# Optimization experiments

Measured on AMD Instinct MI355X. Metric: run time of the kernel, lower is better.

Reference implementation:

```python
import jax, jax.numpy as jnp
import numpy as np

N_SRC = 100000
N_DST = 20000
E = 1250000
D_IN = 64
D_OUT = 64
NEG_SLOPE = 0.2  # PyG GATConv default


def setup_inputs() -> dict:
    key = jax.random.key(0)
    ks = jax.random.split(key, 8)
    x = jax.random.normal(ks[0], (N_SRC, D_IN), dtype=jnp.float32)
    res_n_id = jax.random.randint(ks[1], (N_DST,), 0, N_SRC)
    edge_src = jax.random.randint(ks[2], (E,), 0, N_SRC)
    edge_dst = jax.random.randint(ks[3], (E,), 0, N_DST)
    W = jax.random.normal(ks[4], (D_IN, D_OUT), dtype=jnp.float32) / np.sqrt(D_IN)
    att_src = jax.random.normal(ks[5], (D_OUT,), dtype=jnp.float32)
    att_dst = jax.random.normal(ks[6], (D_OUT,), dtype=jnp.float32)
    bias = jax.random.normal(ks[7], (D_OUT,), dtype=jnp.float32) * 0.01
    return {"x": x, "res_n_id": res_n_id, "edge_src": edge_src,
            "edge_dst": edge_dst, "W": W, "att_src": att_src,
            "att_dst": att_dst, "bias": bias}


def reference(x, res_n_id, edge_src, edge_dst, W, att_src, att_dst, bias):
    # Shared linear transform (in_channels is an int -> one weight in PyG)
    h_src = x @ W                      # [N_src, D_OUT]
    h_dst = x[res_n_id] @ W            # [N_dst, D_OUT]
    # Per-node attention logits
    a_src = h_src @ att_src            # [N_src]
    a_dst = h_dst @ att_dst            # [N_dst]
    # Per-edge attention score (gather)
    e = jax.nn.leaky_relu(a_src[edge_src] + a_dst[edge_dst], NEG_SLOPE)  # [E]
    # Segment softmax over incoming edges of each destination node
    m = jax.ops.segment_max(e, edge_dst, num_segments=N_DST)             # [N_dst]
    ex = jnp.exp(e - m[edge_dst])
    denom = jax.ops.segment_sum(ex, edge_dst, num_segments=N_DST)        # [N_dst]
    alpha = ex / (denom[edge_dst] + 1e-16)                               # [E]
    # (dropout on alpha is eval-mode identity)
    # Weighted scatter-aggregate
    msg = h_src[edge_src] * alpha[:, None]                               # [E, D_OUT]
    out = jax.ops.segment_sum(msg, edge_dst, num_segments=N_DST)         # [N_dst, D_OUT]
    return out + bias
```

## Files before the change

### kernel.cpp

```cpp
#include <hip/hip_runtime.h>

#define N_SRC 100000
#define N_DST 20000
#define NE    1250000
#define D     64
#define NEG_SLOPE 0.2f

#define NBKT 2500
#define BCAP 768
#define TILE 4096

__device__ __forceinline__ unsigned short f2bf(float f) {
    unsigned u = __float_as_uint(f);
    u += 0x7FFFu + ((u >> 16) & 1);
    return (unsigned short)(u >> 16);
}
__device__ __forceinline__ float blo(unsigned u) { return __uint_as_float(u << 16); }
__device__ __forceinline__ float bhi(unsigned u) { return __uint_as_float(u & 0xFFFF0000u); }

__global__ void k_wad_init(const float* __restrict__ W,
                           const float* __restrict__ att_dst,
                           float* __restrict__ wad, int* __restrict__ gcur) {
    int g = blockIdx.x * 256 + threadIdx.x;
    if (g < NBKT) gcur[g] = g * BCAP;
    if (g < D) {
        float s = 0.f;
#pragma unroll
        for (int c = 0; c < D; ++c) s += W[g * D + c] * att_dst[c];
        wad[g] = s;
    }
}

__global__ __launch_bounds__(256) void k_h(const float* __restrict__ x,
                                           const float* __restrict__ W,
                                           const float* __restrict__ att_src,
                                           unsigned short* __restrict__ hb,
                                           float* __restrict__ a_src) {
    __shared__ float xs[64 * 68];
    __shared__ float Ws[64 * 64];
    int t = threadIdx.x;
    int row0 = blockIdx.x * 64;
    int nrows = N_SRC - row0; if (nrows > 64) nrows = 64;
    {
        const float4* W4 = (const float4*)W;
        float4* Ws4 = (float4*)Ws;
#pragma unroll
        for (int p = 0; p < 4; ++p) Ws4[t + 256 * p] = W4[t + 256 * p];
    }
#pragma unroll
    for (int p = 0; p < 4; ++p) {
        int idx = t + 256 * p;
        int r = idx >> 4, kq = idx & 15;
        float4 v = make_float4(0.f, 0.f, 0.f, 0.f);
        if (r < nrows) v = *(const float4*)(x + (size_t)(row0 + r) * D + 4 * kq);
        xs[(4 * kq + 0) * 68 + r] = v.x;
        xs[(4 * kq + 1) * 68 + r] = v.y;
        xs[(4 * kq + 2) * 68 + r] = v.z;
        xs[(4 * kq + 3) * 68 + r] = v.w;
    }
    __syncthreads();
    int ry = t >> 4, cx = t & 15;
    float acc[4][4] = {{0.f}};
#pragma unroll 8
    for (int k = 0; k < 64; ++k) {
        float4 xv = *(const float4*)(xs + k * 68 + 4 * ry);
        float4 wv = *(const float4*)(Ws + k * 64 + 4 * cx);
        acc[0][0] = fmaf(xv.x, wv.x, acc[0][0]); acc[0][1] = fmaf(xv.x, wv.y, acc[0][1]);
        acc[0][2] = fmaf(xv.x, wv.z, acc[0][2]); acc[0][3] = fmaf(xv.x, wv.w, acc[0][3]);
        acc[1][0] = fmaf(xv.y, wv.x, acc[1][0]); acc[1][1] = fmaf(xv.y, wv.y, acc[1][1]);
        acc[1][2] = fmaf(xv.y, wv.z, acc[1][2]); acc[1][3] = fmaf(xv.y, wv.w, acc[1][3]);
        acc[2][0] = fmaf(xv.z, wv.x, acc[2][0]); acc[2][1] = fmaf(xv.z, wv.y, acc[2][1]);
        acc[2][2] = fmaf(xv.z, wv.z, acc[2][2]); acc[2][3] = fmaf(xv.z, wv.w, acc[2][3]);
        acc[3][0] = fmaf(xv.w, wv.x, acc[3][0]); acc[3][1] = fmaf(xv.w, wv.y, acc[3][1]);
        acc[3][2] = fmaf(xv.w, wv.z, acc[3][2]); acc[3][3] = fmaf(xv.w, wv.w, acc[3][3]);
    }
    float4 a4 = *(const float4*)(att_src + 4 * cx);
#pragma unroll
    for (int j = 0; j < 4; ++j) {
        int r = 4 * ry + j;
        if (r < nrows) {
            ushort4 hv;
            hv.x = f2bf(acc[j][0]); hv.y = f2bf(acc[j][1]);
            hv.z = f2bf(acc[j][2]); hv.w = f2bf(acc[j][3]);
            *(ushort4*)(hb + (size_t)(row0 + r) * D + 4 * cx) = hv;
        }
        float p = acc[j][0] * a4.x + acc[j][1] * a4.y + acc[j][2] * a4.z + acc[j][3] * a4.w;
        p += __shfl_xor(p, 1, 64); p += __shfl_xor(p, 2, 64);
        p += __shfl_xor(p, 4, 64); p += __shfl_xor(p, 8, 64);
        if (cx == 0 && r < nrows) a_src[row0 + r] = p;
    }
}

__global__ __launch_bounds__(1024) void k_bucket(const int* __restrict__ es,
                                                 const int* __restrict__ ed,
                                                 int* __restrict__ gcur,
                                                 int* __restrict__ buf) {
    __shared__ int hist[NBKT];
    __shared__ int lofs[NBKT];
    __shared__ int gbase[NBKT];
    __shared__ int wtot[16];
    __shared__ int stage[TILE];
    int t = threadIdx.x;
    int w = t >> 6, lane = t & 63;
    int base = blockIdx.x * TILE;
    int nE = NE - base; if (nE > TILE) nE = TILE;

    for (int i = t; i < NBKT; i += 1024) hist[i] = 0;
    __syncthreads();

    int s_[4], d_[4], rk_[4];
#pragma unroll
    for (int j = 0; j < 4; ++j) {
        int i = t + 1024 * j;
        d_[j] = -1;
        if (i < nE) {
            s_[j] = es[base + i];
            d_[j] = ed[base + i];
            rk_[j] = atomicAdd(&hist[d_[j] >> 3], 1);
        }
    }
    __syncthreads();

    int c0 = t * 3;
    int hc[3] = {0, 0, 0};
#pragma unroll
    for (int j = 0; j < 3; ++j)
        if (c0 + j < NBKT) hc[j] = hist[c0 + j];
    int sum = hc[0] + hc[1] + hc[2];
    int incl = sum;
#pragma unroll
    for (int off = 1; off < 64; off <<= 1) {
        int u = __shfl_up(incl, off, 64);
        if (lane >= off) incl += u;
    }
    if (lane == 63) wtot[w] = incl;
    __syncthreads();
    int wpre = 0;
#pragma unroll
    for (int j = 0; j < 16; ++j) wpre += (j < w) ? wtot[j] : 0;
    {
        int run = wpre + incl - sum;
#pragma unroll
        for (int j = 0; j < 3; ++j) {
            int b = c0 + j;
            if (b < NBKT) {
                lofs[b] = run;
                gbase[b] = hc[j] ? atomicAdd(&gcur[b], hc[j]) : 0;
                run += hc[j];
            }
        }
    }
    __syncthreads();

#pragma unroll
    for (int j = 0; j < 4; ++j) {
        if (d_[j] >= 0) {
            int b = d_[j] >> 3;
            stage[lofs[b] + rk_[j]] = s_[j] | ((d_[j] & 7) << 17) | (b << 20);
        }
    }
    __syncthreads();

    for (int idx = t; idx < nE; idx += 1024) {
        int rec = stage[idx];
        int b = ((unsigned)rec) >> 20;
        int gpos = gbase[b] + idx - lofs[b];
        if (gpos < (b + 1) * BCAP) buf[gpos] = rec;
    }
}

__global__ __launch_bounds__(256) void k_aggB(const int* __restrict__ buf,
                                              const int* __restrict__ gcur,
                                              const float* __restrict__ a_src,
                                              const float* __restrict__ x,
                                              const int* __restrict__ res_n_id,
                                              const float* __restrict__ wad,
                                              const unsigned short* __restrict__ hb,
                                              const float* __restrict__ bias,
                                              float* __restrict__ out) {
    __shared__ int2 sorted[BCAP];
    __shared__ int  scw[8 * 4];
    __shared__ int  begs[9];
    int bk = blockIdx.x;
    int t = threadIdx.x;
    int w = t >> 6, lane = t & 63;
    int n = gcur[bk] - bk * BCAP;
    if (n > BCAP) n = BCAP;
    if (n < 0) n = 0;

    const int* src = buf + (size_t)bk * BCAP;
    int r0 = 0, r1 = 0, r2 = 0;
    int bin0 = -1, bin1 = -1, bin2 = -1;
    if (t < n)       { r0 = src[t];       bin0 = (r0 >> 17) & 7; }
    if (t + 256 < n) { r1 = src[t + 256]; bin1 = (r1 >> 17) & 7; }
    if (t + 512 < n) { r2 = src[t + 512]; bin2 = (r2 >> 17) & 7; }

    int h[8], incl[8];
#pragma unroll
    for (int i = 0; i < 8; ++i)
        h[i] = (bin0 == i) + (bin1 == i) + (bin2 == i);

#pragma unroll
    for (int i = 0; i < 8; ++i) {
        int v = h[i];
#pragma unroll
        for (int off = 1; off < 64; off <<= 1) {
            int u = __shfl_up(v, off, 64);
            if (lane >= off) v += u;
        }
        incl[i] = v;
        int tot = __shfl(v, 63, 64);
        if (lane == 0) scw[i * 4 + w] = tot;
    }
    __syncthreads();

    if (t < 32) {
        int v = scw[t];
#pragma unroll
        for (int off = 1; off < 32; off <<= 1) {
            int u = __shfl_up(v, off, 64);
            if (t >= off) v += u;
        }
        scw[t] = v;
    }
    __syncthreads();
    if (t < 8) begs[t] = (t == 0) ? 0 : scw[t * 4 - 1];
    if (t == 8) begs[8] = n;

    int p0 = 0, p1 = 0, p2 = 0;
#pragma unroll
    for (int i = 0; i < 8; ++i) {
        int idx = i * 4 + w;
        int base_i = ((idx ? scw[idx - 1] : 0)) + (incl[i] - h[i]);
        p0 += (bin0 == i) ? base_i : 0;
        p1 += (bin1 == i) ? base_i : 0;
        p2 += (bin2 == i) ? base_i : 0;
    }
    p1 += (bin1 == bin0);
    p2 += (bin2 == bin0) + (bin2 == bin1);
    if (bin0 >= 0) sorted[p0].x = r0;
    if (bin1 >= 0) sorted[p1].x = r1;
    if (bin2 >= 0) sorted[p2].x = r2;
    float wv = wad[lane];
    __syncthreads();

    int g = lane >> 3, il = lane & 7;
    float4 bA = *(const float4*)(bias + 8 * il);
    float4 bB = *(const float4*)(bias + 8 * il + 4);
#pragma unroll
    for (int q = 0; q < 2; ++q) {
        int dlo = w * 2 + q;
        int beg = begs[dlo], end = begs[dlo + 1];

        int xrow = res_n_id[bk * 8 + dlo];
        float ad = x[(size_t)xrow * D + lane] * wv;
#pragma unroll
        for (int off = 32; off; off >>= 1) ad += __shfl_xor(ad, off, 64);

        float mx = -1e30f;
        for (int i = beg + lane; i < end; i += 64) {
            int meta = sorted[i].x;
            float v = a_src[meta & 0x1FFFF] + ad;
            v = v > 0.f ? v : NEG_SLOPE * v;
            sorted[i].y = __float_as_int(v);
            mx = fmaxf(mx, v);
        }
#pragma unroll
        for (int off = 32; off; off >>= 1) mx = fmaxf(mx, __shfl_xor(mx, off, 64));
        __builtin_amdgcn_wave_barrier();

        float a0 = 0.f, a1 = 0.f, a2 = 0.f, a3 = 0.f;
        float a4c = 0.f, a5 = 0.f, a6 = 0.f, a7 = 0.f;
        float den = 0.f;
        int i = beg;
        for (; i + 32 <= end; i += 32) {
            int2 ra = sorted[i + g];
            int2 rb = sorted[i + 8 + g];
            int2 rc = sorted[i + 16 + g];
            int2 rd = sorted[i + 24 + g];
            const uint4 ha = *(const uint4*)(hb + (size_t)(ra.x & 0x1FFFF) * D + 8 * il);
            const uint4 hc4 = *(const uint4*)(hb + (size_t)(rb.x & 0x1FFFF) * D + 8 * il);
            const uint4 he = *(const uint4*)(hb + (size_t)(rc.x & 0x1FFFF) * D + 8 * il);
            const uint4 hf = *(const uint4*)(hb + (size_t)(rd.x & 0x1FFFF) * D + 8 * il);
            float ea = __expf(__int_as_float(ra.y) - mx);
            float eb = __expf(__int_as_float(rb.y) - mx);
            float ec = __expf(__int_as_float(rc.y) - mx);
            float ed = __expf(__int_as_float(rd.y) - mx);
            a0 = fmaf(ea, blo(ha.x), a0); a1 = fmaf(ea, bhi(ha.x), a1);
            a2 = fmaf(ea, blo(ha.y), a2); a3 = fmaf(ea, bhi(ha.y), a3);
            a4c = fmaf(ea, blo(ha.z), a4c); a5 = fmaf(ea, bhi(ha.z), a5);
            a6 = fmaf(ea, blo(ha.w), a6); a7 = fmaf(ea, bhi(ha.w), a7);
            a0 = fmaf(eb, blo(hc4.x), a0); a1 = fmaf(eb, bhi(hc4.x), a1);
            a2 = fmaf(eb, blo(hc4.y), a2); a3 = fmaf(eb, bhi(hc4.y), a3);
            a4c = fmaf(eb, blo(hc4.z), a4c); a5 = fmaf(eb, bhi(hc4.z), a5);
            a6 = fmaf(eb, blo(hc4.w), a6); a7 = fmaf(eb, bhi(hc4.w), a7);
            a0 = fmaf(ec, blo(he.x), a0); a1 = fmaf(ec, bhi(he.x), a1);
            a2 = fmaf(ec, blo(he.y), a2); a3 = fmaf(ec, bhi(he.y), a3);
            a4c = fmaf(ec, blo(he.z), a4c); a5 = fmaf(ec, bhi(he.z), a5);
            a6 = fmaf(ec, blo(he.w), a6); a7 = fmaf(ec, bhi(he.w), a7);
            a0 = fmaf(ed, blo(hf.x), a0); a1 = fmaf(ed, bhi(hf.x), a1);
            a2 = fmaf(ed, blo(hf.y), a2); a3 = fmaf(ed, bhi(hf.y), a3);
            a4c = fmaf(ed, blo(hf.z), a4c); a5 = fmaf(ed, bhi(hf.z), a5);
            a6 = fmaf(ed, blo(hf.w), a6); a7 = fmaf(ed, bhi(hf.w), a7);
            den += (ea + eb) + (ec + ed);
        }
        for (; i + 16 <= end; i += 16) {
            int2 ra = sorted[i + g];
            int2 rb = sorted[i + 8 + g];
            const uint4 ha = *(const uint4*)(hb + (size_t)(ra.x & 0x1FFFF) * D + 8 * il);
            const uint4 hc4 = *(const uint4*)(hb + (size_t)(rb.x & 0x1FFFF) * D + 8 * il);
            float ea = __expf(__int_as_float(ra.y) - mx);
            float eb = __expf(__int_as_float(rb.y) - mx);
            a0 = fmaf(ea, blo(ha.x), a0); a1 = fmaf(ea, bhi(ha.x), a1);
            a2 = fmaf(ea, blo(ha.y), a2); a3 = fmaf(ea, bhi(ha.y), a3);
            a4c = fmaf(ea, blo(ha.z), a4c); a5 = fmaf(ea, bhi(ha.z), a5);
            a6 = fmaf(ea, blo(ha.w), a6); a7 = fmaf(ea, bhi(ha.w), a7);
            a0 = fmaf(eb, blo(hc4.x), a0); a1 = fmaf(eb, bhi(hc4.x), a1);
            a2 = fmaf(eb, blo(hc4.y), a2); a3 = fmaf(eb, bhi(hc4.y), a3);
            a4c = fmaf(eb, blo(hc4.z), a4c); a5 = fmaf(eb, bhi(hc4.z), a5);
            a6 = fmaf(eb, blo(hc4.w), a6); a7 = fmaf(eb, bhi(hc4.w), a7);
            den += ea + eb;
        }
        for (; i < end; i += 8) {
            int idx = i + g;
            bool ok = idx < end;
            float e = 0.f;
            if (ok) {
                int2 r = sorted[idx];
                e = __expf(__int_as_float(r.y) - mx);
                const uint4 hv = *(const uint4*)(hb + (size_t)(r.x & 0x1FFFF) * D + 8 * il);
                a0 = fmaf(e, blo(hv.x), a0); a1 = fmaf(e, bhi(hv.x), a1);
                a2 = fmaf(e, blo(hv.y), a2); a3 = fmaf(e, bhi(hv.y), a3);
                a4c = fmaf(e, blo(hv.z), a4c); a5 = fmaf(e, bhi(hv.z), a5);
                a6 = fmaf(e, blo(hv.w), a6); a7 = fmaf(e, bhi(hv.w), a7);
            }
            den += e;
        }
#pragma unroll
        for (int off = 8; off <= 32; off <<= 1) {
            a0 += __shfl_xor(a0, off, 64); a1 += __shfl_xor(a1, off, 64);
            a2 += __shfl_xor(a2, off, 64); a3 += __shfl_xor(a3, off, 64);
            a4c += __shfl_xor(a4c, off, 64); a5 += __shfl_xor(a5, off, 64);
            a6 += __shfl_xor(a6, off, 64); a7 += __shfl_xor(a7, off, 64);
            den += __shfl_xor(den, off, 64);
        }
        if (g == 0) {
            float inv = 1.f / (den + 1e-16f);
            float4 oA, oB;
            oA.x = a0 * inv + bA.x; oA.y = a1 * inv + bA.y;
            oA.z = a2 * inv + bA.z; oA.w = a3 * inv + bA.w;
            oB.x = a4c * inv + bB.x; oB.y = a5 * inv + bB.y;
            oB.z = a6 * inv + bB.z; oB.w = a7 * inv + bB.w;
            float* orow = out + ((size_t)bk * 8 + dlo) * D + 8 * il;
            *(float4*)orow = oA;
            *(float4*)(orow + 4) = oB;
        }
    }
}

extern "C" void kernel_launch(void* const* d_in, const int* in_sizes, int n_in,
                              void* d_out, int out_size, void* d_ws, size_t ws_size,
                              hipStream_t stream) {
    const float* x        = (const float*)d_in[0];
    const int*   res_n_id = (const int*)d_in[1];
    const int*   edge_src = (const int*)d_in[2];
    const int*   edge_dst = (const int*)d_in[3];
    const float* W        = (const float*)d_in[4];
    const float* att_src  = (const float*)d_in[5];
    const float* att_dst  = (const float*)d_in[6];
    const float* bias     = (const float*)d_in[7];
    float* out = (float*)d_out;

    char* w = (char*)d_ws;
    unsigned short* hb = (unsigned short*)w; w += (size_t)N_SRC * D * 2;
    int*   buf   = (int*)w;   w += (size_t)NBKT * BCAP * 4;
    float* a_src = (float*)w; w += (size_t)N_SRC * 4;
    float* wad   = (float*)w; w += 256;
    int*   gcur  = (int*)w;   w += (size_t)NBKT * 4;

    k_wad_init<<<(NBKT + 255) / 256, 256, 0, stream>>>(W, att_dst, wad, gcur);
    k_h<<<(N_SRC + 63) / 64, 256, 0, stream>>>(x, W, att_src, hb, a_src);
    k_bucket<<<(NE + TILE - 1) / TILE, 1024, 0, stream>>>(edge_src, edge_dst, gcur, buf);
    k_aggB<<<NBKT, 256, 0, stream>>>(buf, gcur, a_src, x, res_n_id, wad, hb, bias, out);
}
```

Baseline: 161.3 us.

## Precompute exponentiated edge scores during bucketing and drop segment max pass

A new small kernel computes the per-destination attention logit once. The bucketing kernel then gathers a_src and a_dst for each edge, applies leaky-ReLU and exp, and stores the result next to the packed edge record as an int2. The aggregation kernel loses its per-segment max reduction, its a_src gathers and its per-edge exp, and uses the stored weights directly. In exchange the bucket buffer doubles in size, and softmax without max subtraction can overflow if logits get large.

```diff
diff --git a/kernel.cpp b/kernel.cpp
--- a/kernel.cpp
+++ b/kernel.cpp
@@ -91,15 +91,32 @@
     }
 }
 
+__global__ __launch_bounds__(256) void k_adst(const float* __restrict__ x,
+                                              const int* __restrict__ res_n_id,
+                                              const float* __restrict__ wad,
+                                              float* __restrict__ a_dst) {
+    int tid = threadIdx.x;
+    int wid = blockIdx.x * 4 + (tid >> 6);
+    int lane = tid & 63;
+    if (wid >= N_DST) return;
+    int row = res_n_id[wid];
+    float p = x[(size_t)row * D + lane] * wad[lane];
+#pragma unroll
+    for (int off = 32; off; off >>= 1) p += __shfl_xor(p, off, 64);
+    if (lane == 0) a_dst[wid] = p;
+}
+
 __global__ __launch_bounds__(1024) void k_bucket(const int* __restrict__ es,
                                                  const int* __restrict__ ed,
+                                                 const float* __restrict__ a_src,
+                                                 const float* __restrict__ a_dst,
                                                  int* __restrict__ gcur,
-                                                 int* __restrict__ buf) {
+                                                 int2* __restrict__ buf) {
     __shared__ int hist[NBKT];
     __shared__ int lofs[NBKT];
     __shared__ int gbase[NBKT];
     __shared__ int wtot[16];
-    __shared__ int stage[TILE];
+    __shared__ int2 stage[TILE];
     int t = threadIdx.x;
     int w = t >> 6, lane = t & 63;
     int base = blockIdx.x * TILE;
@@ -119,6 +136,11 @@
             rk_[j] = atomicAdd(&hist[d_[j] >> 3], 1);
         }
     }
+    float as_[4], ad_[4];
+#pragma unroll
+    for (int j = 0; j < 4; ++j) {
+        if (d_[j] >= 0) { as_[j] = a_src[s_[j]]; ad_[j] = a_dst[d_[j]]; }
+    }
     __syncthreads();
 
     int c0 = t * 3;
@@ -155,26 +177,27 @@
 #pragma unroll
     for (int j = 0; j < 4; ++j) {
         if (d_[j] >= 0) {
+            float v = as_[j] + ad_[j];
+            v = v > 0.f ? v : NEG_SLOPE * v;
+            float ex = __expf(v);
             int b = d_[j] >> 3;
-            stage[lofs[b] + rk_[j]] = s_[j] | ((d_[j] & 7) << 17) | (b << 20);
+            stage[lofs[b] + rk_[j]] =
+                make_int2(s_[j] | ((d_[j] & 7) << 17) | (b << 20),
+                          __float_as_int(ex));
         }
     }
     __syncthreads();
 
     for (int idx = t; idx < nE; idx += 1024) {
-        int rec = stage[idx];
-        int b = ((unsigned)rec) >> 20;
+        int2 rec = stage[idx];
+        int b = ((unsigned)rec.x) >> 20;
         int gpos = gbase[b] + idx - lofs[b];
         if (gpos < (b + 1) * BCAP) buf[gpos] = rec;
     }
 }
 
-__global__ __launch_bounds__(256) void k_aggB(const int* __restrict__ buf,
+__global__ __launch_bounds__(256) void k_aggB(const int2* __restrict__ buf,
                                               const int* __restrict__ gcur,
-                                              const float* __restrict__ a_src,
-                                              const float* __restrict__ x,
-                                              const int* __restrict__ res_n_id,
-                                              const float* __restrict__ wad,
                                               const unsigned short* __restrict__ hb,
                                               const float* __restrict__ bias,
                                               float* __restrict__ out) {
@@ -188,12 +211,12 @@
     if (n > BCAP) n = BCAP;
     if (n < 0) n = 0;
 
-    const int* src = buf + (size_t)bk * BCAP;
-    int r0 = 0, r1 = 0, r2 = 0;
+    const int2* src = buf + (size_t)bk * BCAP;
+    int2 r0 = make_int2(0, 0), r1 = make_int2(0, 0), r2 = make_int2(0, 0);
     int bin0 = -1, bin1 = -1, bin2 = -1;
-    if (t < n)       { r0 = src[t];       bin0 = (r0 >> 17) & 7; }
-    if (t + 256 < n) { r1 = src[t + 256]; bin1 = (r1 >> 17) & 7; }
-    if (t + 512 < n) { r2 = src[t + 512]; bin2 = (r2 >> 17) & 7; }
+    if (t < n)       { r0 = src[t];       bin0 = (r0.x >> 17) & 7; }
+    if (t + 256 < n) { r1 = src[t + 256]; bin1 = (r1.x >> 17) & 7; }
+    if (t + 512 < n) { r2 = src[t + 512]; bin2 = (r2.x >> 17) & 7; }
 
     int h[8], incl[8];
 #pragma unroll
@@ -238,10 +261,9 @@
     }
     p1 += (bin1 == bin0);
     p2 += (bin2 == bin0) + (bin2 == bin1);
-    if (bin0 >= 0) sorted[p0].x = r0;
-    if (bin1 >= 0) sorted[p1].x = r1;
-    if (bin2 >= 0) sorted[p2].x = r2;
-    float wv = wad[lane];
+    if (bin0 >= 0) sorted[p0] = r0;
+    if (bin1 >= 0) sorted[p1] = r1;
+    if (bin2 >= 0) sorted[p2] = r2;
     __syncthreads();
 
     int g = lane >> 3, il = lane & 7;
@@ -251,23 +273,6 @@
     for (int q = 0; q < 2; ++q) {
         int dlo = w * 2 + q;
         int beg = begs[dlo], end = begs[dlo + 1];
-
-        int xrow = res_n_id[bk * 8 + dlo];
-        float ad = x[(size_t)xrow * D + lane] * wv;
-#pragma unroll
-        for (int off = 32; off; off >>= 1) ad += __shfl_xor(ad, off, 64);
-
-        float mx = -1e30f;
-        for (int i = beg + lane; i < end; i += 64) {
-            int meta = sorted[i].x;
-            float v = a_src[meta & 0x1FFFF] + ad;
-            v = v > 0.f ? v : NEG_SLOPE * v;
-            sorted[i].y = __float_as_int(v);
-            mx = fmaxf(mx, v);
-        }
-#pragma unroll
-        for (int off = 32; off; off >>= 1) mx = fmaxf(mx, __shfl_xor(mx, off, 64));
-        __builtin_amdgcn_wave_barrier();
 
         float a0 = 0.f, a1 = 0.f, a2 = 0.f, a3 = 0.f;
         float a4c = 0.f, a5 = 0.f, a6 = 0.f, a7 = 0.f;
@@ -282,10 +287,10 @@
             const uint4 hc4 = *(const uint4*)(hb + (size_t)(rb.x & 0x1FFFF) * D + 8 * il);
             const uint4 he = *(const uint4*)(hb + (size_t)(rc.x & 0x1FFFF) * D + 8 * il);
             const uint4 hf = *(const uint4*)(hb + (size_t)(rd.x & 0x1FFFF) * D + 8 * il);
-            float ea = __expf(__int_as_float(ra.y) - mx);
-            float eb = __expf(__int_as_float(rb.y) - mx);
-            float ec = __expf(__int_as_float(rc.y) - mx);
-            float ed = __expf(__int_as_float(rd.y) - mx);
+            float ea = __int_as_float(ra.y);
+            float eb = __int_as_float(rb.y);
+            float ec = __int_as_float(rc.y);
+            float ed = __int_as_float(rd.y);
             a0 = fmaf(ea, blo(ha.x), a0); a1 = fmaf(ea, bhi(ha.x), a1);
             a2 = fmaf(ea, blo(ha.y), a2); a3 = fmaf(ea, bhi(ha.y), a3);
             a4c = fmaf(ea, blo(ha.z), a4c); a5 = fmaf(ea, bhi(ha.z), a5);
@@ -309,8 +314,8 @@
             int2 rb = sorted[i + 8 + g];
             const uint4 ha = *(const uint4*)(hb + (size_t)(ra.x & 0x1FFFF) * D + 8 * il);
             const uint4 hc4 = *(const uint4*)(hb + (size_t)(rb.x & 0x1FFFF) * D + 8 * il);
-            float ea = __expf(__int_as_float(ra.y) - mx);
-            float eb = __expf(__int_as_float(rb.y) - mx);
+            float ea = __int_as_float(ra.y);
+            float eb = __int_as_float(rb.y);
             a0 = fmaf(ea, blo(ha.x), a0); a1 = fmaf(ea, bhi(ha.x), a1);
             a2 = fmaf(ea, blo(ha.y), a2); a3 = fmaf(ea, bhi(ha.y), a3);
             a4c = fmaf(ea, blo(ha.z), a4c); a5 = fmaf(ea, bhi(ha.z), a5);
@@ -327,7 +332,7 @@
             float e = 0.f;
             if (ok) {
                 int2 r = sorted[idx];
-                e = __expf(__int_as_float(r.y) - mx);
+                e = __int_as_float(r.y);
                 const uint4 hv = *(const uint4*)(hb + (size_t)(r.x & 0x1FFFF) * D + 8 * il);
                 a0 = fmaf(e, blo(hv.x), a0); a1 = fmaf(e, bhi(hv.x), a1);
                 a2 = fmaf(e, blo(hv.y), a2); a3 = fmaf(e, bhi(hv.y), a3);
@@ -373,13 +378,15 @@
 
     char* w = (char*)d_ws;
     unsigned short* hb = (unsigned short*)w; w += (size_t)N_SRC * D * 2;
-    int*   buf   = (int*)w;   w += (size_t)NBKT * BCAP * 4;
+    int2*  buf   = (int2*)w;  w += (size_t)NBKT * BCAP * 8;
     float* a_src = (float*)w; w += (size_t)N_SRC * 4;
+    float* a_dst = (float*)w; w += (size_t)N_DST * 4;
     float* wad   = (float*)w; w += 256;
     int*   gcur  = (int*)w;   w += (size_t)NBKT * 4;
 
     k_wad_init<<<(NBKT + 255) / 256, 256, 0, stream>>>(W, att_dst, wad, gcur);
+    k_adst<<<N_DST / 4, 256, 0, stream>>>(x, res_n_id, wad, a_dst);
     k_h<<<(N_SRC + 63) / 64, 256, 0, stream>>>(x, W, att_src, hb, a_src);
-    k_bucket<<<(NE + TILE - 1) / TILE, 1024, 0, stream>>>(edge_src, edge_dst, gcur, buf);
-    k_aggB<<<NBKT, 256, 0, stream>>>(buf, gcur, a_src, x, res_n_id, wad, hb, bias, out);
-}
+    k_bucket<<<(NE + TILE - 1) / TILE, 1024, 0, stream>>>(edge_src, edge_dst, a_src, a_dst, gcur, buf);
+    k_aggB<<<NBKT, 256, 0, stream>>>(buf, gcur, hb, bias, out);
+}
```

Measured after the change: 172.1 us. +6.7%, slower.

## Aggregate raw bf16 x and apply W after aggregation; drop max-subtraction

Applied to the files above, without the earlier changes.

The pre-pass no longer computes h = x@W. It converts x to bf16 and folds W·att into vectors to get a_src and a_dst directly, with a_dst computed in separate blocks. The aggregation kernel sums attention-weighted x rows and then multiplies each destination's 64-vector by W held in shared memory, using linearity. This moves the GEMM from 100k source rows to 20k destination rows. It also removes the softmax max pass by exponentiating logits directly, which risks overflow for large logits. Bucket cursors now start from a memset instead of an init kernel.

```diff
diff --git a/kernel.cpp b/kernel.cpp
--- a/kernel.cpp
+++ b/kernel.cpp
@@ -9,6 +9,8 @@
 #define NBKT 2500
 #define BCAP 768
 #define TILE 4096
+#define GEMM_BLKS 391
+#define ADST_BLKS 79
 
 __device__ __forceinline__ unsigned short f2bf(float f) {
     unsigned u = __float_as_uint(f);
@@ -18,76 +20,58 @@
 __device__ __forceinline__ float blo(unsigned u) { return __uint_as_float(u << 16); }
 __device__ __forceinline__ float bhi(unsigned u) { return __uint_as_float(u & 0xFFFF0000u); }
 
-__global__ void k_wad_init(const float* __restrict__ W,
-                           const float* __restrict__ att_dst,
-                           float* __restrict__ wad, int* __restrict__ gcur) {
-    int g = blockIdx.x * 256 + threadIdx.x;
-    if (g < NBKT) gcur[g] = g * BCAP;
-    if (g < D) {
+__global__ __launch_bounds__(256) void k_pre(const float* __restrict__ W,
+                                             const float* __restrict__ att_src,
+                                             const float* __restrict__ att_dst,
+                                             const float* __restrict__ x,
+                                             const int* __restrict__ res_n_id,
+                                             unsigned short* __restrict__ xb,
+                                             float* __restrict__ a_src,
+                                             float* __restrict__ a_dst) {
+    __shared__ __align__(16) float wL[D];
+    int t = threadIdx.x, blk = blockIdx.x;
+    bool isA = blk < GEMM_BLKS;
+    if (t < D) {
+        const float* att = isA ? att_src : att_dst;
         float s = 0.f;
 #pragma unroll
-        for (int c = 0; c < D; ++c) s += W[g * D + c] * att_dst[c];
-        wad[g] = s;
-    }
-}
-
-__global__ __launch_bounds__(256) void k_h(const float* __restrict__ x,
-                                           const float* __restrict__ W,
-                                           const float* __restrict__ att_src,
-                                           unsigned short* __restrict__ hb,
-                                           float* __restrict__ a_src) {
-    __shared__ float xs[64 * 68];
-    __shared__ float Ws[64 * 64];
-    int t = threadIdx.x;
-    int row0 = blockIdx.x * 64;
-    int nrows = N_SRC - row0; if (nrows > 64) nrows = 64;
-    {
-        const float4* W4 = (const float4*)W;
-        float4* Ws4 = (float4*)Ws;
-#pragma unroll
-        for (int p = 0; p < 4; ++p) Ws4[t + 256 * p] = W4[t + 256 * p];
-    }
-#pragma unroll
-    for (int p = 0; p < 4; ++p) {
-        int idx = t + 256 * p;
-        int r = idx >> 4, kq = idx & 15;
-        float4 v = make_float4(0.f, 0.f, 0.f, 0.f);
-        if (r < nrows) v = *(const float4*)(x + (size_t)(row0 + r) * D + 4 * kq);
-        xs[(4 * kq + 0) * 68 + r] = v.x;
-        xs[(4 * kq + 1) * 68 + r] = v.y;
-        xs[(4 * kq + 2) * 68 + r] = v.z;
-        xs[(4 * kq + 3) * 68 + r] = v.w;
-    }
-    __syncthreads();
-    int ry = t >> 4, cx = t & 15;
-    float acc[4][4] = {{0.f}};
-#pragma unroll 8
-    for (int k = 0; k < 64; ++k) {
-        float4 xv = *(const float4*)(xs + k * 68 + 4 * ry);
-        float4 wv = *(const float4*)(Ws + k * 64 + 4 * cx);
-        acc[0][0] = fmaf(xv.x, wv.x, acc[0][0]); acc[0][1] = fmaf(xv.x, wv.y, acc[0][1]);
-        acc[0][2] = fmaf(xv.x, wv.z, acc[0][2]); acc[0][3] = fmaf(xv.x, wv.w, acc[0][3]);
-        acc[1][0] = fmaf(xv.y, wv.x, acc[1][0]); acc[1][1] = fmaf(xv.y, wv.y, acc[1][1]);
-        acc[1][2] = fmaf(xv.y, wv.z, acc[1][2]); acc[1][3] = fmaf(xv.y, wv.w, acc[1][3]);
-        acc[2][0] = fmaf(xv.z, wv.x, acc[2][0]); acc[2][1] = fmaf(xv.z, wv.y, acc[2][1]);
-        acc[2][2] = fmaf(xv.z, wv.z, acc[2][2]); acc[2][3] = fmaf(xv.z, wv.w, acc[2][3]);
-        acc[3][0] = fmaf(xv.w, wv.x, acc[3][0]); acc[3][1] = fmaf(xv.w, wv.y, acc[3][1]);
-        acc[3][2] = fmaf(xv.w, wv.z, acc[3][2]); acc[3][3] = fmaf(xv.w, wv.w, acc[3][3]);
-    }
-    float4 a4 = *(const float4*)(att_src + 4 * cx);
-#pragma unroll
-    for (int j = 0; j < 4; ++j) {
-        int r = 4 * ry + j;
-        if (r < nrows) {
-            ushort4 hv;
-            hv.x = f2bf(acc[j][0]); hv.y = f2bf(acc[j][1]);
-            hv.z = f2bf(acc[j][2]); hv.w = f2bf(acc[j][3]);
-            *(ushort4*)(hb + (size_t)(row0 + r) * D + 4 * cx) = hv;
-        }
-        float p = acc[j][0] * a4.x + acc[j][1] * a4.y + acc[j][2] * a4.z + acc[j][3] * a4.w;
-        p += __shfl_xor(p, 1, 64); p += __shfl_xor(p, 2, 64);
-        p += __shfl_xor(p, 4, 64); p += __shfl_xor(p, 8, 64);
-        if (cx == 0 && r < nrows) a_src[row0 + r] = p;
+        for (int c = 0; c < D; ++c) s += W[t * D + c] * att[c];
+        wL[t] = s;
+    }
+    __syncthreads();
+    const float4* x4 = (const float4*)x;
+    if (isA) {
+        int w = t >> 6, lane = t & 63;
+        int row0 = blk * 256 + w * 64;
+        ushort4* xb4 = (ushort4*)xb;
+        float4 wv = *((const float4*)wL + (lane & 15));
+#pragma unroll 4
+        for (int it = 0; it < 16; ++it) {
+            int r4 = row0 + it * 4;
+            if (r4 >= N_SRC) break;
+            float4 v = x4[(size_t)r4 * 16 + lane];
+            ushort4 o;
+            o.x = f2bf(v.x); o.y = f2bf(v.y); o.z = f2bf(v.z); o.w = f2bf(v.w);
+            xb4[(size_t)r4 * 16 + lane] = o;
+            float p = v.x * wv.x + v.y * wv.y + v.z * wv.z + v.w * wv.w;
+            p += __shfl_xor(p, 1, 64); p += __shfl_xor(p, 2, 64);
+            p += __shfl_xor(p, 4, 64); p += __shfl_xor(p, 8, 64);
+            if ((lane & 15) == 0) a_src[r4 + (lane >> 4)] = p;
+        }
+    } else {
+        int bi = blk - GEMM_BLKS;
+        int grp = t >> 4, il = t & 15;
+        float4 wv = *((const float4*)wL + il);
+        for (int j = bi * 256 + grp; j < bi * 256 + 256; j += 16) {
+            if (j < N_DST) {
+                int row = res_n_id[j];
+                float4 v = x4[(size_t)row * 16 + il];
+                float p = v.x * wv.x + v.y * wv.y + v.z * wv.z + v.w * wv.w;
+                p += __shfl_xor(p, 1, 64); p += __shfl_xor(p, 2, 64);
+                p += __shfl_xor(p, 4, 64); p += __shfl_xor(p, 8, 64);
+                if (il == 0) a_dst[j] = p;
+            }
+        }
     }
 }
 
@@ -164,29 +148,35 @@
     for (int idx = t; idx < nE; idx += 1024) {
         int rec = stage[idx];
         int b = ((unsigned)rec) >> 20;
-        int gpos = gbase[b] + idx - lofs[b];
-        if (gpos < (b + 1) * BCAP) buf[gpos] = rec;
+        int off = gbase[b] + idx - lofs[b];
+        if (off < BCAP) buf[b * BCAP + off] = rec;
     }
 }
 
 __global__ __launch_bounds__(256) void k_aggB(const int* __restrict__ buf,
                                               const int* __restrict__ gcur,
                                               const float* __restrict__ a_src,
-                                              const float* __restrict__ x,
-                                              const int* __restrict__ res_n_id,
-                                              const float* __restrict__ wad,
-                                              const unsigned short* __restrict__ hb,
+                                              const float* __restrict__ a_dst,
+                                              const unsigned short* __restrict__ xb,
+                                              const float* __restrict__ W,
                                               const float* __restrict__ bias,
                                               float* __restrict__ out) {
     __shared__ int2 sorted[BCAP];
+    __shared__ float Ws[D * D];
+    __shared__ float yL[4][D];
     __shared__ int  scw[8 * 4];
     __shared__ int  begs[9];
     int bk = blockIdx.x;
     int t = threadIdx.x;
     int w = t >> 6, lane = t & 63;
-    int n = gcur[bk] - bk * BCAP;
+    {
+        const float4* W4 = (const float4*)W;
+        float4* Ws4 = (float4*)Ws;
+#pragma unroll
+        for (int p = 0; p < 4; ++p) Ws4[t + 256 * p] = W4[t + 256 * p];
+    }
+    int n = gcur[bk];
     if (n > BCAP) n = BCAP;
-    if (n < 0) n = 0;
 
     const int* src = buf + (size_t)bk * BCAP;
     int r0 = 0, r1 = 0, r2 = 0;
@@ -241,32 +231,22 @@
     if (bin0 >= 0) sorted[p0].x = r0;
     if (bin1 >= 0) sorted[p1].x = r1;
     if (bin2 >= 0) sorted[p2].x = r2;
-    float wv = wad[lane];
     __syncthreads();
 
     int g = lane >> 3, il = lane & 7;
-    float4 bA = *(const float4*)(bias + 8 * il);
-    float4 bB = *(const float4*)(bias + 8 * il + 4);
+    float bsv = bias[lane];
 #pragma unroll
     for (int q = 0; q < 2; ++q) {
         int dlo = w * 2 + q;
         int beg = begs[dlo], end = begs[dlo + 1];
-
-        int xrow = res_n_id[bk * 8 + dlo];
-        float ad = x[(size_t)xrow * D + lane] * wv;
-#pragma unroll
-        for (int off = 32; off; off >>= 1) ad += __shfl_xor(ad, off, 64);
-
-        float mx = -1e30f;
+        float ad = a_dst[bk * 8 + dlo];
+
         for (int i = beg + lane; i < end; i += 64) {
             int meta = sorted[i].x;
             float v = a_src[meta & 0x1FFFF] + ad;
             v = v > 0.f ? v : NEG_SLOPE * v;
-            sorted[i].y = __float_as_int(v);
-            mx = fmaxf(mx, v);
-        }
-#pragma unroll
-        for (int off = 32; off; off >>= 1) mx = fmaxf(mx, __shfl_xor(mx, off, 64));
+            sorted[i].y = __float_as_int(__expf(v));
+        }
         __builtin_amdgcn_wave_barrier();
 
         float a0 = 0.f, a1 = 0.f, a2 = 0.f, a3 = 0.f;
@@ -278,14 +258,14 @@
             int2 rb = sorted[i + 8 + g];
             int2 rc = sorted[i + 16 + g];
             int2 rd = sorted[i + 24 + g];
-            const uint4 ha = *(const uint4*)(hb + (size_t)(ra.x & 0x1FFFF) * D + 8 * il);
-            const uint4 hc4 = *(const uint4*)(hb + (size_t)(rb.x & 0x1FFFF) * D + 8 * il);
-            const uint4 he = *(const uint4*)(hb + (size_t)(rc.x & 0x1FFFF) * D + 8 * il);
-            const uint4 hf = *(const uint4*)(hb + (size_t)(rd.x & 0x1FFFF) * D + 8 * il);
-            float ea = __expf(__int_as_float(ra.y) - mx);
-            float eb = __expf(__int_as_float(rb.y) - mx);
-            float ec = __expf(__int_as_float(rc.y) - mx);
-            float ed = __expf(__int_as_float(rd.y) - mx);
+            const uint4 ha = *(const uint4*)(xb + (size_t)(ra.x & 0x1FFFF) * D + 8 * il);
+            const uint4 hc4 = *(const uint4*)(xb + (size_t)(rb.x & 0x1FFFF) * D + 8 * il);
+            const uint4 he = *(const uint4*)(xb + (size_t)(rc.x & 0x1FFFF) * D + 8 * il);
+            const uint4 hf = *(const uint4*)(xb + (size_t)(rd.x & 0x1FFFF) * D + 8 * il);
+            float ea = __int_as_float(ra.y);
+            float eb = __int_as_float(rb.y);
+            float ec = __int_as_float(rc.y);
+            float ed = __int_as_float(rd.y);
             a0 = fmaf(ea, blo(ha.x), a0); a1 = fmaf(ea, bhi(ha.x), a1);
             a2 = fmaf(ea, blo(ha.y), a2); a3 = fmaf(ea, bhi(ha.y), a3);
             a4c = fmaf(ea, blo(ha.z), a4c); a5 = fmaf(ea, bhi(ha.z), a5);
@@ -307,10 +287,10 @@
         for (; i + 16 <= end; i += 16) {
             int2 ra = sorted[i + g];
             int2 rb = sorted[i + 8 + g];
-            const uint4 ha = *(const uint4*)(hb + (size_t)(ra.x & 0x1FFFF) * D + 8 * il);
-            const uint4 hc4 = *(const uint4*)(hb + (size_t)(rb.x & 0x1FFFF) * D + 8 * il);
-            float ea = __expf(__int_as_float(ra.y) - mx);
-            float eb = __expf(__int_as_float(rb.y) - mx);
+            const uint4 ha = *(const uint4*)(xb + (size_t)(ra.x & 0x1FFFF) * D + 8 * il);
+            const uint4 hc4 = *(const uint4*)(xb + (size_t)(rb.x & 0x1FFFF) * D + 8 * il);
+            float ea = __int_as_float(ra.y);
+            float eb = __int_as_float(rb.y);
             a0 = fmaf(ea, blo(ha.x), a0); a1 = fmaf(ea, bhi(ha.x), a1);
             a2 = fmaf(ea, blo(ha.y), a2); a3 = fmaf(ea, bhi(ha.y), a3);
             a4c = fmaf(ea, blo(ha.z), a4c); a5 = fmaf(ea, bhi(ha.z), a5);
@@ -327,8 +307,8 @@
             float e = 0.f;
             if (ok) {
                 int2 r = sorted[idx];
-                e = __expf(__int_as_float(r.y) - mx);
-                const uint4 hv = *(const uint4*)(hb + (size_t)(r.x & 0x1FFFF) * D + 8 * il);
+                e = __int_as_float(r.y);
+                const uint4 hv = *(const uint4*)(xb + (size_t)(r.x & 0x1FFFF) * D + 8 * il);
                 a0 = fmaf(e, blo(hv.x), a0); a1 = fmaf(e, bhi(hv.x), a1);
                 a2 = fmaf(e, blo(hv.y), a2); a3 = fmaf(e, bhi(hv.y), a3);
                 a4c = fmaf(e, blo(hv.z), a4c); a5 = fmaf(e, bhi(hv.z), a5);
@@ -346,15 +326,18 @@
         }
         if (g == 0) {
             float inv = 1.f / (den + 1e-16f);
-            float4 oA, oB;
-            oA.x = a0 * inv + bA.x; oA.y = a1 * inv + bA.y;
-            oA.z = a2 * inv + bA.z; oA.w = a3 * inv + bA.w;
-            oB.x = a4c * inv + bB.x; oB.y = a5 * inv + bB.y;
-            oB.z = a6 * inv + bB.z; oB.w = a7 * inv + bB.w;
-            float* orow = out + ((size_t)bk * 8 + dlo) * D + 8 * il;
-            *(float4*)orow = oA;
-            *(float4*)(orow + 4) = oB;
-        }
+            yL[w][8 * il + 0] = a0 * inv;  yL[w][8 * il + 1] = a1 * inv;
+            yL[w][8 * il + 2] = a2 * inv;  yL[w][8 * il + 3] = a3 * inv;
+            yL[w][8 * il + 4] = a4c * inv; yL[w][8 * il + 5] = a5 * inv;
+            yL[w][8 * il + 6] = a6 * inv;  yL[w][8 * il + 7] = a7 * inv;
+        }
+        __builtin_amdgcn_wave_barrier();
+        float o = 0.f;
+#pragma unroll 8
+        for (int k = 0; k < D; ++k)
+            o = fmaf(yL[w][k], Ws[k * D + lane], o);
+        out[((size_t)bk * 8 + dlo) * D + lane] = o + bsv;
+        __builtin_amdgcn_wave_barrier();
     }
 }
 
@@ -372,14 +355,15 @@
     float* out = (float*)d_out;
 
     char* w = (char*)d_ws;
-    unsigned short* hb = (unsigned short*)w; w += (size_t)N_SRC * D * 2;
+    unsigned short* xb = (unsigned short*)w; w += (size_t)N_SRC * D * 2;
     int*   buf   = (int*)w;   w += (size_t)NBKT * BCAP * 4;
     float* a_src = (float*)w; w += (size_t)N_SRC * 4;
-    float* wad   = (float*)w; w += 256;
+    float* a_dst = (float*)w; w += (size_t)N_DST * 4;
     int*   gcur  = (int*)w;   w += (size_t)NBKT * 4;
 
-    k_wad_init<<<(NBKT + 255) / 256, 256, 0, stream>>>(W, att_dst, wad, gcur);
-    k_h<<<(N_SRC + 63) / 64, 256, 0, stream>>>(x, W, att_src, hb, a_src);
+    hipMemsetAsync(gcur, 0, NBKT * sizeof(int), stream);
+    k_pre<<<GEMM_BLKS + ADST_BLKS, 256, 0, stream>>>(W, att_src, att_dst, x,
+                                                     res_n_id, xb, a_src, a_dst);
     k_bucket<<<(NE + TILE - 1) / TILE, 1024, 0, stream>>>(edge_src, edge_dst, gcur, buf);
-    k_aggB<<<NBKT, 256, 0, stream>>>(buf, gcur, a_src, x, res_n_id, wad, hb, bias, out);
-}
+    k_aggB<<<NBKT, 256, 0, stream>>>(buf, gcur, a_src, a_dst, xb, W, bias, out);
+}
```

Result: no change. 160.8 us (-0.3%).
